# Kernel optimization log

Hardware: AMD Instinct MI355X
Metric: run time of the kernel (lower is better)

## Reference

```python
import jax, jax.numpy as jnp
import numpy as np

N = 100_000   # nodes
E = 1_600_000 # edges
G = 128       # graphs in batch
DIN, DOUT = 100, 200


def setup_inputs() -> dict:
    key = jax.random.key(0)
    ks = jax.random.split(key, 12)
    def lin_w(k, fan_in, fan_out):
        return (jax.random.normal(k, (fan_in, fan_out), jnp.float32) / np.sqrt(fan_in)).astype(jnp.float32)
    return {
        "x": jax.random.normal(ks[0], (N, DIN), jnp.float32),
        "edge_index": jax.random.randint(ks[1], (2, E), 0, N, dtype=jnp.int32),
        "batch": jnp.sort(jax.random.randint(ks[2], (N,), 0, G, dtype=jnp.int32)),
        "W1": lin_w(ks[3], DIN, DOUT),  "b1": jnp.zeros((DOUT,), jnp.float32),
        "Wc": lin_w(ks[4], DOUT, DOUT), "bc": jnp.zeros((DOUT,), jnp.float32),
        "W2": lin_w(ks[5], DOUT, DOUT), "b2": jnp.zeros((DOUT,), jnp.float32),
        "W3": lin_w(ks[6], DOUT, DOUT), "b3": jnp.zeros((DOUT,), jnp.float32),
        "Wcls": lin_w(ks[7], DOUT, 2),  "bcls": jnp.zeros((2,), jnp.float32),
    }


def gcn_conv(x, W, b, src, dst, n_nodes):
    """PyG GCNConv: D^{-1/2}(A+I)D^{-1/2} X W + b, symmetric norm with self-loops."""
    h = x @ W  # [N, Dout]
    # degree at targets including the self-loop (+1)
    deg = jax.ops.segment_sum(jnp.ones((src.shape[0],), x.dtype), dst, num_segments=n_nodes) + 1.0
    dinv = jax.lax.rsqrt(deg)  # [N]
    # gather -> normalize -> scatter-add (messages along edges)
    msg = h[src] * (dinv[src] * dinv[dst])[:, None]          # [E, Dout]
    agg = jax.ops.segment_sum(msg, dst, num_segments=n_nodes)  # [N, Dout]
    # self-loop contribution handled analytically: norm_ii = dinv[i]^2
    agg = agg + h * (dinv * dinv)[:, None]
    return agg + b


def reference(x, edge_index, batch, W1, b1, Wc, bc, W2, b2, W3, b3, Wcls, bcls):
    src, dst = edge_index[0], edge_index[1]
    h = jax.nn.relu(gcn_conv(x, W1, b1, src, dst, N))
    # dropout is identity at eval time
    h = h @ Wc + bc
    h = jax.nn.relu(gcn_conv(h, W2, b2, src, dst, N))
    h = gcn_conv(h, W3, b3, src, dst, N)
    pooled = jax.ops.segment_max(h, batch, num_segments=G)  # global max pool -> [G, Dout]
    logits = pooled @ Wcls + bcls
    return jax.nn.softmax(logits, axis=1)
```

## Files before the change

### kernel.cpp

```cpp
#include <hip/hip_runtime.h>
#include <stdint.h>

#define N_NODES 100000
#define N_EDGES 1600000
#define N_GRAPHS 128
#define DIN 100
#define DOUT 200
#define LDH 200
#define LDX 128

#define NB 391
#define BCAP 5120
#define EPB 2048

typedef unsigned short u16;
typedef unsigned int u32;
typedef _Float16 f16;
typedef f16 half8 __attribute__((ext_vector_type(8)));
typedef f16 half4 __attribute__((ext_vector_type(4)));
typedef f16 half2v __attribute__((ext_vector_type(2)));
typedef float floatx4 __attribute__((ext_vector_type(4)));

__device__ __forceinline__ float h2f(u16 h) {
  f16 x; __builtin_memcpy(&x, &h, 2); return (float)x;
}
__device__ __forceinline__ u16 f2h(float f) {
  f16 x = (f16)f; u16 r; __builtin_memcpy(&r, &x, 2); return r;
}

__device__ __forceinline__ void pack_frag(const float* __restrict__ W, int K, int nfrag,
                                          u16* __restrict__ out, int idx) {
  if (idx >= nfrag) return;
  int lane = idx & 63;
  int t = idx >> 6;
  int ct = t % 13, ks = t / 13;
  int n = ct * 16 + (lane & 15);
  int kbase = ks * 32 + (lane >> 4) * 8;
  u16 v[8];
  #pragma unroll
  for (int j = 0; j < 8; ++j) {
    int k = kbase + j;
    float f = (k < K && n < DOUT) ? W[(size_t)k * DOUT + n] : 0.f;
    v[j] = f2h(f);
  }
  uint4 o;
  o.x = (u32)v[0] | ((u32)v[1] << 16);
  o.y = (u32)v[2] | ((u32)v[3] << 16);
  o.z = (u32)v[4] | ((u32)v[5] << 16);
  o.w = (u32)v[6] | ((u32)v[7] << 16);
  *(uint4*)(out + (size_t)idx * 8) = o;
}

#define B_GB    391
#define B_COMB  549
#define B_PK1   562
#define B_PK3   585
#define B_TOT   587
__global__ void k_prep(const int* __restrict__ batch, int* __restrict__ gstart,
                       int* __restrict__ gend, int* __restrict__ gcur,
                       const float* __restrict__ Wc, const float* __restrict__ bc,
                       const float* __restrict__ W2, float* __restrict__ Wc2,
                       float* __restrict__ bc2, const float* __restrict__ W1,
                       const float* __restrict__ W3, u16* __restrict__ Wpk1,
                       u16* __restrict__ Wpk3) {
  int b = blockIdx.x, t = threadIdx.x;
  if (b < B_GB) {
    int i = b * 256 + t;
    if (i >= N_NODES) return;
    int g = batch[i];
    if (i == 0 || batch[i - 1] != g) gstart[g] = i;
    if (i == N_NODES - 1 || batch[i + 1] != g) gend[g] = i;
  } else if (b < B_COMB) {
    int gid = (b - B_GB) * 256 + t;
    if (gid >= 201 * DOUT) return;
    int r = gid / DOUT, c = gid % DOUT;
    const float* a = (r < DOUT) ? (Wc + (size_t)r * DOUT) : bc;
    float s = 0.f;
    for (int k = 0; k < DOUT; ++k) s += a[k] * W2[(size_t)k * DOUT + c];
    if (r < DOUT) Wc2[(size_t)r * DOUT + c] = s;
    else bc2[c] = s;
  } else if (b < B_PK1) {
    pack_frag(W1, DIN, 4 * 13 * 64, Wpk1, (b - B_COMB) * 256 + t);
  } else if (b < B_PK3) {
    pack_frag(W3, DOUT, 7 * 13 * 64, Wpk3, (b - B_PK1) * 256 + t);
  } else {
    int i = (b - B_PK3) * 256 + t;
    if (i < NB) gcur[i] = 0;
  }
}

__global__ void k_bucket(const int* __restrict__ src, const int* __restrict__ dst,
                         int* __restrict__ gcur, uint2* __restrict__ ebuf, int E) {
  __shared__ int hist[NB];
  __shared__ int base[NB];
  __shared__ int cur[NB];
  int t = threadIdx.x;
  int e0 = blockIdx.x * EPB;
  int e1 = min(e0 + EPB, E);
  for (int j = t; j < NB; j += 256) { hist[j] = 0; cur[j] = 0; }
  __syncthreads();
  for (int i = e0 + t; i < e1; i += 256)
    atomicAdd(&hist[dst[i] >> 8], 1);
  __syncthreads();
  for (int j = t; j < NB; j += 256)
    base[j] = hist[j] ? atomicAdd(&gcur[j], hist[j]) : 0;
  __syncthreads();
  for (int i = e0 + t; i < e1; i += 256) {
    int d = dst[i];
    int b = d >> 8;
    int off = atomicAdd(&cur[b], 1);
    int pos = base[b] + off;
    if (pos < BCAP)
      ebuf[(size_t)b * BCAP + pos] = make_uint2((u32)d, (u32)src[i]);
  }
}

__global__ void k_csr(const uint2* __restrict__ ebuf, const int* __restrict__ gcur,
                      int* __restrict__ rowptr, float* __restrict__ dinv,
                      int* __restrict__ colv) {
  __shared__ int s_cnt[256];
  __shared__ int s_cur[256];
  __shared__ int s_scan[256];
  __shared__ int s_g[NB];
  __shared__ int s_base;
  int b = blockIdx.x, t = threadIdx.x;
  for (int j = t; j < NB; j += 256) s_g[j] = gcur[j];
  s_cnt[t] = 0;
  __syncthreads();
  if (t == 0) {
    int run = 0;
    for (int i = 0; i < b; ++i) run += s_g[i];
    s_base = run;
    if (b == NB - 1) rowptr[N_NODES] = run + s_g[b];
  }
  __syncthreads();
  int cnt = s_g[b];
  int base = s_base;
  int node0 = b << 8;
  const uint2* eb = ebuf + (size_t)b * BCAP;
  for (int i = t; i < cnt; i += 256)
    atomicAdd(&s_cnt[eb[i].x & 255], 1);
  __syncthreads();
  int v = s_cnt[t];
  s_scan[t] = v;
  __syncthreads();
  for (int o = 1; o < 256; o <<= 1) {
    int x = (t >= o) ? s_scan[t - o] : 0;
    __syncthreads();
    s_scan[t] += x;
    __syncthreads();
  }
  int run = s_scan[t] - v;
  s_cur[t] = base + run;
  int node = node0 + t;
  if (node < N_NODES) {
    rowptr[node] = base + run;
    dinv[node] = rsqrtf((float)v + 1.0f);
  }
  __syncthreads();
  for (int i = t; i < cnt; i += 256) {
    uint2 e = eb[i];
    int pos = atomicAdd(&s_cur[e.x & 255], 1);
    colv[pos] = (int)e.y;
  }
}

#define P_XS  25000
#define P_TOT 25023
__global__ void k_post(const float* __restrict__ x, const float* __restrict__ dinv,
                       u16* __restrict__ xs, const float* __restrict__ Wc2,
                       u16* __restrict__ Wpk2) {
  int b = blockIdx.x, t = threadIdx.x;
  if (b < P_XS) {
    int gid = b * 256 + t;
    int node = gid >> 6, lane = gid & 63;
    if (node >= N_NODES) return;
    if (lane >= 50) {
      int c = 100 + (lane - 50) * 2;
      *(half2v*)(xs + (size_t)node * LDX + c) = half2v{0, 0};
      return;
    }
    float d = dinv[node];
    float2 vv = *(const float2*)(x + (size_t)node * DIN + lane * 2);
    half2v o; o[0] = (f16)(d * vv.x); o[1] = (f16)(d * vv.y);
    *(half2v*)(xs + (size_t)node * LDX + lane * 2) = o;
  } else {
    pack_frag(Wc2, DOUT, 7 * 13 * 64, Wpk2, (b - P_XS) * 256 + t);
  }
}

template <int NKS>
__global__ __launch_bounds__(256) void k_gemm_mfma(const u16* __restrict__ A, int lda,
                                                   const u16* __restrict__ Wpk,
                                                   const float* __restrict__ bias,
                                                   const float* __restrict__ rowscale,
                                                   u16* __restrict__ C, int relu, int nrows) {
  int wv = threadIdx.x >> 6;
  int lane = threadIdx.x & 63;
  int r0 = blockIdx.x * 128 + wv * 32;
  int m = lane & 15, q = lane >> 4;
  int row0 = r0 + m, row1 = r0 + 16 + m;
  bool ok0 = (row0 < nrows), ok1 = (row1 < nrows);
  const u16* a0p = A + (size_t)row0 * lda + q * 8;
  const u16* a1p = A + (size_t)row1 * lda + q * 8;

  floatx4 acc0[13], acc1[13];
  #pragma unroll
  for (int ct = 0; ct < 13; ++ct) {
    acc0[ct] = floatx4{0.f, 0.f, 0.f, 0.f};
    acc1[ct] = floatx4{0.f, 0.f, 0.f, 0.f};
  }

  const u16* wp = Wpk + (size_t)lane * 8;
  #pragma unroll
  for (int ks = 0; ks < NKS; ++ks) {
    half8 a0 = ok0 ? *(const half8*)(a0p + ks * 32) : half8{0, 0, 0, 0, 0, 0, 0, 0};
    half8 a1 = ok1 ? *(const half8*)(a1p + ks * 32) : half8{0, 0, 0, 0, 0, 0, 0, 0};
    #pragma unroll
    for (int ct = 0; ct < 13; ++ct) {
      half8 bfr = *(const half8*)(wp + (size_t)(ks * 13 + ct) * 512);
      acc0[ct] = __builtin_amdgcn_mfma_f32_16x16x32_f16(a0, bfr, acc0[ct], 0, 0, 0);
      acc1[ct] = __builtin_amdgcn_mfma_f32_16x16x32_f16(a1, bfr, acc1[ct], 0, 0, 0);
    }
  }

  float sc0[4], sc1[4];
  #pragma unroll
  for (int rg = 0; rg < 4; ++rg) {
    int or0 = r0 + q * 4 + rg;
    int or1 = r0 + 16 + q * 4 + rg;
    sc0[rg] = (rowscale && or0 < nrows) ? rowscale[or0] : 1.f;
    sc1[rg] = (rowscale && or1 < nrows) ? rowscale[or1] : 1.f;
  }

  #pragma unroll
  for (int ct = 0; ct < 13; ++ct) {
    int c = ct * 16 + m;
    if (c >= DOUT) continue;
    float bv = bias ? bias[c] : 0.f;
    #pragma unroll
    for (int rg = 0; rg < 4; ++rg) {
      int or0 = r0 + q * 4 + rg;
      if (or0 < nrows) {
        float v = acc0[ct][rg] + bv;
        if (relu) v = fmaxf(v, 0.f);
        C[(size_t)or0 * LDH + c] = f2h(v * sc0[rg]);
      }
      int or1 = r0 + 16 + q * 4 + rg;
      if (or1 < nrows) {
        float v = acc1[ct][rg] + bv;
        if (relu) v = fmaxf(v, 0.f);
        C[(size_t)or1 * LDH + c] = f2h(v * sc1[rg]);
      }
    }
  }
}

__global__ void k_agg200h(const u16* __restrict__ T, const float* __restrict__ dinv,
                          const int* __restrict__ rowptr, const int* __restrict__ col,
                          const float* __restrict__ bias, u16* __restrict__ OUT,
                          int relu) {
  int wave = (blockIdx.x * blockDim.x + threadIdx.x) >> 6;
  int lane = threadIdx.x & 63;
  if (wave >= N_NODES || lane >= 50) return;
  int node = wave;
  int c4 = lane * 4;
  float ax = 0.f, ay = 0.f, az = 0.f, aw = 0.f;
  int beg = rowptr[node], end = rowptr[node + 1];
  int e = beg;
  for (; e + 8 <= end; e += 8) {
    int s[8];
    half4 tv[8];
    #pragma unroll
    for (int j = 0; j < 8; ++j) s[j] = col[e + j];
    #pragma unroll
    for (int j = 0; j < 8; ++j)
      tv[j] = *(const half4*)(T + (size_t)s[j] * LDH + c4);
    #pragma unroll
    for (int j = 0; j < 8; ++j) {
      ax += (float)tv[j][0];
      ay += (float)tv[j][1];
      az += (float)tv[j][2];
      aw += (float)tv[j][3];
    }
  }
  for (; e < end; ++e) {
    half4 tv = *(const half4*)(T + (size_t)col[e] * LDH + c4);
    ax += (float)tv[0]; ay += (float)tv[1];
    az += (float)tv[2]; aw += (float)tv[3];
  }
  float di = dinv[node];
  half4 sv = *(const half4*)(T + (size_t)node * LDH + c4);
  float rx = di * (ax + (float)sv[0]);
  float ry = di * (ay + (float)sv[1]);
  float rz = di * (az + (float)sv[2]);
  float rw = di * (aw + (float)sv[3]);
  if (bias) {
    rx += bias[c4 + 0]; ry += bias[c4 + 1];
    rz += bias[c4 + 2]; rw += bias[c4 + 3];
  }
  if (relu) {
    rx = fmaxf(rx, 0.f); ry = fmaxf(ry, 0.f);
    rz = fmaxf(rz, 0.f); rw = fmaxf(rw, 0.f);
  }
  half4 o;
  o[0] = (f16)rx; o[1] = (f16)ry; o[2] = (f16)rz; o[3] = (f16)rw;
  *(half4*)(OUT + (size_t)node * LDH + c4) = o;
}

__global__ void k_agg100h(const u16* __restrict__ T, const float* __restrict__ dinv,
                          const int* __restrict__ rowptr, const int* __restrict__ col,
                          u16* __restrict__ OUT) {
  int wave = (blockIdx.x * blockDim.x + threadIdx.x) >> 6;
  int lane = threadIdx.x & 63;
  if (wave >= N_NODES) return;
  int node = wave;
  if (lane >= 50) {
    int c = 100 + (lane - 50) * 2;
    *(half2v*)(OUT + (size_t)node * LDX + c) = half2v{0, 0};
    return;
  }
  int c2 = lane * 2;
  float ax = 0.f, ay = 0.f;
  int beg = rowptr[node], end = rowptr[node + 1];
  int e = beg;
  for (; e + 8 <= end; e += 8) {
    int s[8];
    half2v tv[8];
    #pragma unroll
    for (int j = 0; j < 8; ++j) s[j] = col[e + j];
    #pragma unroll
    for (int j = 0; j < 8; ++j)
      tv[j] = *(const half2v*)(T + (size_t)s[j] * LDX + c2);
    #pragma unroll
    for (int j = 0; j < 8; ++j) {
      ax += (float)tv[j][0];
      ay += (float)tv[j][1];
    }
  }
  for (; e < end; ++e) {
    half2v tv = *(const half2v*)(T + (size_t)col[e] * LDX + c2);
    ax += (float)tv[0]; ay += (float)tv[1];
  }
  float di = dinv[node];
  half2v sv = *(const half2v*)(T + (size_t)node * LDX + c2);
  half2v o;
  o[0] = (f16)(di * (ax + (float)sv[0]));
  o[1] = (f16)(di * (ay + (float)sv[1]));
  *(half2v*)(OUT + (size_t)node * LDX + c2) = o;
}

#define POOL_CHUNKS 8
__global__ void k_pool1h(const u16* __restrict__ H, const int* __restrict__ gstart,
                         const int* __restrict__ gend, float* __restrict__ part) {
  int g = blockIdx.x, c = blockIdx.y, t = threadIdx.x;
  if (t >= DOUT) return;
  int s = gstart[g], e = gend[g];
  float m = -3.4e38f;
  if (s >= 0 && e >= s && e < N_NODES) {
    int len = e - s + 1;
    int cs = s + (int)(((long long)len * c) / POOL_CHUNKS);
    int ce = s + (int)(((long long)len * (c + 1)) / POOL_CHUNKS);
    for (int i = cs; i < ce; ++i) m = fmaxf(m, h2f(H[(size_t)i * LDH + t]));
  }
  part[(size_t)(g * POOL_CHUNKS + c) * DOUT + t] = m;
}

__global__ void k_poolcls(const float* __restrict__ part, const float* __restrict__ Wcls,
                          const float* __restrict__ bcls, float* __restrict__ out) {
  __shared__ float l0s[256], l1s[256];
  int g = blockIdx.x, t = threadIdx.x;
  float c0 = 0.f, c1 = 0.f;
  if (t < DOUT) {
    float m = -3.4e38f;
    #pragma unroll
    for (int c = 0; c < POOL_CHUNKS; ++c)
      m = fmaxf(m, part[(size_t)(g * POOL_CHUNKS + c) * DOUT + t]);
    c0 = m * Wcls[t * 2 + 0];
    c1 = m * Wcls[t * 2 + 1];
  }
  l0s[t] = c0; l1s[t] = c1;
  __syncthreads();
  for (int o = 128; o > 0; o >>= 1) {
    if (t < o) { l0s[t] += l0s[t + o]; l1s[t] += l1s[t + o]; }
    __syncthreads();
  }
  if (t == 0) {
    float l0 = l0s[0] + bcls[0], l1 = l1s[0] + bcls[1];
    float m = fmaxf(l0, l1);
    float e0 = expf(l0 - m), e1 = expf(l1 - m);
    float inv = 1.0f / (e0 + e1);
    out[g * 2 + 0] = e0 * inv;
    out[g * 2 + 1] = e1 * inv;
  }
}

static inline size_t align256(size_t x) { return (x + 255) & ~(size_t)255; }

extern "C" void kernel_launch(void* const* d_in, const int* in_sizes, int n_in,
                              void* d_out, int out_size, void* d_ws, size_t ws_size,
                              hipStream_t stream) {
  const float* x     = (const float*)d_in[0];
  const int*   ei    = (const int*)d_in[1];
  const int*   batch = (const int*)d_in[2];
  const float* W1    = (const float*)d_in[3];
  const float* b1    = (const float*)d_in[4];
  const float* Wc    = (const float*)d_in[5];
  const float* bc    = (const float*)d_in[6];
  const float* W2    = (const float*)d_in[7];
  const float* b2    = (const float*)d_in[8];
  const float* W3    = (const float*)d_in[9];
  const float* b3    = (const float*)d_in[10];
  const float* Wcls  = (const float*)d_in[11];
  const float* bcls  = (const float*)d_in[12];
  float* out = (float*)d_out;

  const int N = N_NODES, E = N_EDGES;
  const int* src = ei;
  const int* dst = ei + E;

  char* ws = (char*)d_ws;
  size_t off = 0;
  float* dinv   = (float*)(ws + off); off = align256(off + (size_t)N * 4);
  int*   rowptr = (int*)  (ws + off); off = align256(off + (size_t)(N + 1) * 4);
  int*   col    = (int*)  (ws + off); off = align256(off + (size_t)E * 4);
  int*   gcur   = (int*)  (ws + off); off = align256(off + (size_t)NB * 4);
  int*   gstart = (int*)  (ws + off); off = align256(off + 512);
  int*   gend   = (int*)  (ws + off); off = align256(off + 512);
  float* Wc2    = (float*)(ws + off); off = align256(off + (size_t)DOUT * DOUT * 4);
  float* bc2    = (float*)(ws + off); off = align256(off + (size_t)DOUT * 4);
  u16*   Wpk1   = (u16*)  (ws + off); off = align256(off + (size_t)4 * 13 * 64 * 8 * 2);
  u16*   Wpk2   = (u16*)  (ws + off); off = align256(off + (size_t)7 * 13 * 64 * 8 * 2);
  u16*   Wpk3   = (u16*)  (ws + off); off = align256(off + (size_t)7 * 13 * 64 * 8 * 2);
  u16*   xs     = (u16*)  (ws + off); off = align256(off + ((size_t)N * LDX + 128) * 2);
  u16*   bufX   = (u16*)  (ws + off); off = align256(off + ((size_t)N * LDX + 128) * 2);
  u16*   buf0   = (u16*)  (ws + off); off = align256(off + ((size_t)N * LDH + 128) * 2);
  u16*   buf1   = (u16*)  (ws + off); off = align256(off + ((size_t)N * LDH + 128) * 2);
  u16*   buf2   = (u16*)  (ws + off); off = align256(off + ((size_t)N * LDH + 128) * 2);

  uint2* ebuf = (uint2*)buf0;
  float* part = (float*)buf1;

  k_prep<<<B_TOT, 256, 0, stream>>>(batch, gstart, gend, gcur,
                                    Wc, bc, W2, Wc2, bc2, W1, W3, Wpk1, Wpk3);
  k_bucket<<<(E + EPB - 1) / EPB, 256, 0, stream>>>(src, dst, gcur, ebuf, E);
  k_csr<<<NB, 256, 0, stream>>>(ebuf, gcur, rowptr, dinv, col);
  k_post<<<P_TOT, 256, 0, stream>>>(x, dinv, xs, Wc2, Wpk2);

  int gemmb = (N + 127) / 128;
  int aggb  = (N + 3) / 4;

  k_agg100h<<<aggb, 256, 0, stream>>>(xs, dinv, rowptr, col, bufX);
  k_gemm_mfma<4><<<gemmb, 256, 0, stream>>>(bufX, LDX, Wpk1, b1, nullptr, buf0, 1, N);
  k_gemm_mfma<7><<<gemmb, 256, 0, stream>>>(buf0, LDH, Wpk2, bc2, dinv, buf2, 0, N);
  k_agg200h<<<aggb, 256, 0, stream>>>(buf2, dinv, rowptr, col, b2, buf0, 1);
  k_gemm_mfma<7><<<gemmb, 256, 0, stream>>>(buf0, LDH, Wpk3, nullptr, dinv, buf1, 0, N);
  k_agg200h<<<aggb, 256, 0, stream>>>(buf1, dinv, rowptr, col, b3, buf2, 0);

  dim3 pg(N_GRAPHS, POOL_CHUNKS);
  k_pool1h<<<pg, 256, 0, stream>>>(buf2, gstart, gend, part);
  k_poolcls<<<N_GRAPHS, 256, 0, stream>>>(part, Wcls, bcls, out);
}
```

Baseline: 681.1 us.

## Replace atomic bucket offsets with per-block histogram scan for deterministic edge bucketing

The edge-bucketing step is split into three phases. Per-block histograms are folded into the prep kernel, a new scan kernel computes exclusive offsets per bucket across blocks, and a scatter kernel writes edges at those offsets. This removes the global atomicAdd on bucket counters and makes edge order within buckets deterministic. In exchange it adds an extra launch, a column-strided scan over histAll, and a second read of dst.

After: 679.5 us. No clear change (-0.2%).

```diff
diff --git a/kernel.cpp b/kernel.cpp
--- a/kernel.cpp
+++ b/kernel.cpp
@@ -12,6 +12,7 @@
 #define NB 391
 #define BCAP 5120
 #define EPB 2048
+#define NBLK 782
 
 typedef unsigned short u16;
 typedef unsigned int u32;
@@ -55,9 +56,10 @@
 #define B_COMB  549
 #define B_PK1   562
 #define B_PK3   585
-#define B_TOT   587
+#define B_TOT   (585 + NBLK)
 __global__ void k_prep(const int* __restrict__ batch, int* __restrict__ gstart,
-                       int* __restrict__ gend, int* __restrict__ gcur,
+                       int* __restrict__ gend, const int* __restrict__ dst,
+                       int* __restrict__ histAll,
                        const float* __restrict__ Wc, const float* __restrict__ bc,
                        const float* __restrict__ W2, float* __restrict__ Wc2,
                        float* __restrict__ bc2, const float* __restrict__ W1,
@@ -84,34 +86,57 @@
   } else if (b < B_PK3) {
     pack_frag(W3, DOUT, 7 * 13 * 64, Wpk3, (b - B_PK1) * 256 + t);
   } else {
-    int i = (b - B_PK3) * 256 + t;
-    if (i < NB) gcur[i] = 0;
-  }
-}
-
-__global__ void k_bucket(const int* __restrict__ src, const int* __restrict__ dst,
-                         int* __restrict__ gcur, uint2* __restrict__ ebuf, int E) {
-  __shared__ int hist[NB];
-  __shared__ int base[NB];
+    __shared__ int hist[NB];
+    int hb = b - B_PK3;
+    int e0 = hb * EPB;
+    int e1 = min(e0 + EPB, N_EDGES);
+    for (int j = t; j < NB; j += 256) hist[j] = 0;
+    __syncthreads();
+    for (int i = e0 + t; i < e1; i += 256)
+      atomicAdd(&hist[dst[i] >> 8], 1);
+    __syncthreads();
+    for (int j = t; j < NB; j += 256)
+      histAll[(size_t)hb * NB + j] = hist[j];
+  }
+}
+
+__global__ void k_scan(const int* __restrict__ histAll, int* __restrict__ baseAll,
+                       int* __restrict__ gcur) {
+  __shared__ int s[256];
+  int j = blockIdx.x, t = threadIdx.x;
+  int run = 0;
+  for (int c = 0; c < NBLK; c += 256) {
+    int idx = c + t;
+    int v = (idx < NBLK) ? histAll[(size_t)idx * NB + j] : 0;
+    s[t] = v;
+    __syncthreads();
+    for (int o = 1; o < 256; o <<= 1) {
+      int x = (t >= o) ? s[t - o] : 0;
+      __syncthreads();
+      s[t] += x;
+      __syncthreads();
+    }
+    if (idx < NBLK) baseAll[(size_t)idx * NB + j] = run + s[t] - v;
+    run += s[255];
+    __syncthreads();
+  }
+  if (t == 0) gcur[j] = run;
+}
+
+__global__ void k_scatter(const int* __restrict__ src, const int* __restrict__ dst,
+                          const int* __restrict__ baseAll, uint2* __restrict__ ebuf) {
   __shared__ int cur[NB];
-  int t = threadIdx.x;
-  int e0 = blockIdx.x * EPB;
-  int e1 = min(e0 + EPB, E);
-  for (int j = t; j < NB; j += 256) { hist[j] = 0; cur[j] = 0; }
-  __syncthreads();
-  for (int i = e0 + t; i < e1; i += 256)
-    atomicAdd(&hist[dst[i] >> 8], 1);
-  __syncthreads();
-  for (int j = t; j < NB; j += 256)
-    base[j] = hist[j] ? atomicAdd(&gcur[j], hist[j]) : 0;
+  int b = blockIdx.x, t = threadIdx.x;
+  int e0 = b * EPB;
+  int e1 = min(e0 + EPB, N_EDGES);
+  for (int j = t; j < NB; j += 256) cur[j] = baseAll[(size_t)b * NB + j];
   __syncthreads();
   for (int i = e0 + t; i < e1; i += 256) {
     int d = dst[i];
-    int b = d >> 8;
-    int off = atomicAdd(&cur[b], 1);
-    int pos = base[b] + off;
+    int bk = d >> 8;
+    int pos = atomicAdd(&cur[bk], 1);
     if (pos < BCAP)
-      ebuf[(size_t)b * BCAP + pos] = make_uint2((u32)d, (u32)src[i]);
+      ebuf[(size_t)bk * BCAP + pos] = make_uint2((u32)d, (u32)src[i]);
   }
 }
 
@@ -421,29 +446,32 @@
 
   char* ws = (char*)d_ws;
   size_t off = 0;
-  float* dinv   = (float*)(ws + off); off = align256(off + (size_t)N * 4);
-  int*   rowptr = (int*)  (ws + off); off = align256(off + (size_t)(N + 1) * 4);
-  int*   col    = (int*)  (ws + off); off = align256(off + (size_t)E * 4);
-  int*   gcur   = (int*)  (ws + off); off = align256(off + (size_t)NB * 4);
-  int*   gstart = (int*)  (ws + off); off = align256(off + 512);
-  int*   gend   = (int*)  (ws + off); off = align256(off + 512);
-  float* Wc2    = (float*)(ws + off); off = align256(off + (size_t)DOUT * DOUT * 4);
-  float* bc2    = (float*)(ws + off); off = align256(off + (size_t)DOUT * 4);
-  u16*   Wpk1   = (u16*)  (ws + off); off = align256(off + (size_t)4 * 13 * 64 * 8 * 2);
-  u16*   Wpk2   = (u16*)  (ws + off); off = align256(off + (size_t)7 * 13 * 64 * 8 * 2);
-  u16*   Wpk3   = (u16*)  (ws + off); off = align256(off + (size_t)7 * 13 * 64 * 8 * 2);
-  u16*   xs     = (u16*)  (ws + off); off = align256(off + ((size_t)N * LDX + 128) * 2);
-  u16*   bufX   = (u16*)  (ws + off); off = align256(off + ((size_t)N * LDX + 128) * 2);
-  u16*   buf0   = (u16*)  (ws + off); off = align256(off + ((size_t)N * LDH + 128) * 2);
-  u16*   buf1   = (u16*)  (ws + off); off = align256(off + ((size_t)N * LDH + 128) * 2);
-  u16*   buf2   = (u16*)  (ws + off); off = align256(off + ((size_t)N * LDH + 128) * 2);
+  float* dinv    = (float*)(ws + off); off = align256(off + (size_t)N * 4);
+  int*   rowptr  = (int*)  (ws + off); off = align256(off + (size_t)(N + 1) * 4);
+  int*   col     = (int*)  (ws + off); off = align256(off + (size_t)E * 4);
+  int*   gcur    = (int*)  (ws + off); off = align256(off + (size_t)NB * 4);
+  int*   histAll = (int*)  (ws + off); off = align256(off + (size_t)NBLK * NB * 4);
+  int*   baseAll = (int*)  (ws + off); off = align256(off + (size_t)NBLK * NB * 4);
+  int*   gstart  = (int*)  (ws + off); off = align256(off + 512);
+  int*   gend    = (int*)  (ws + off); off = align256(off + 512);
+  float* Wc2     = (float*)(ws + off); off = align256(off + (size_t)DOUT * DOUT * 4);
+  float* bc2     = (float*)(ws + off); off = align256(off + (size_t)DOUT * 4);
+  u16*   Wpk1    = (u16*)  (ws + off); off = align256(off + (size_t)4 * 13 * 64 * 8 * 2);
+  u16*   Wpk2    = (u16*)  (ws + off); off = align256(off + (size_t)7 * 13 * 64 * 8 * 2);
+  u16*   Wpk3    = (u16*)  (ws + off); off = align256(off + (size_t)7 * 13 * 64 * 8 * 2);
+  u16*   xs      = (u16*)  (ws + off); off = align256(off + ((size_t)N * LDX + 128) * 2);
+  u16*   bufX    = (u16*)  (ws + off); off = align256(off + ((size_t)N * LDX + 128) * 2);
+  u16*   buf0    = (u16*)  (ws + off); off = align256(off + ((size_t)N * LDH + 128) * 2);
+  u16*   buf1    = (u16*)  (ws + off); off = align256(off + ((size_t)N * LDH + 128) * 2);
+  u16*   buf2    = (u16*)  (ws + off); off = align256(off + ((size_t)N * LDH + 128) * 2);
 
   uint2* ebuf = (uint2*)buf0;
   float* part = (float*)buf1;
 
-  k_prep<<<B_TOT, 256, 0, stream>>>(batch, gstart, gend, gcur,
+  k_prep<<<B_TOT, 256, 0, stream>>>(batch, gstart, gend, dst, histAll,
                                     Wc, bc, W2, Wc2, bc2, W1, W3, Wpk1, Wpk3);
-  k_bucket<<<(E + EPB - 1) / EPB, 256, 0, stream>>>(src, dst, gcur, ebuf, E);
+  k_scan<<<NB, 256, 0, stream>>>(histAll, baseAll, gcur);
+  k_scatter<<<NBLK, 256, 0, stream>>>(src, dst, baseAll, ebuf);
   k_csr<<<NB, 256, 0, stream>>>(ebuf, gcur, rowptr, dinv, col);
   k_post<<<P_TOT, 256, 0, stream>>>(x, dinv, xs, Wc2, Wpk2);
 
```
